# Kernel tuning notes

Hardware: AMD Instinct MI355X
Metric: run time of the kernel (lower is better)

The kernel has to match this reference:

```python
import jax, jax.numpy as jnp
import numpy as np

ATTN = 128

def _gelu(x):
    return jax.nn.gelu(x, approximate=False)

def _mlp3(x, W1, b1, W2, b2, W3, b3):
    h = _gelu(x @ W1.T + b1)
    h = _gelu(h @ W2.T + b2)
    return h @ W3.T + b3

def setup_inputs() -> dict:
    key = jax.random.key(0)
    ks = jax.random.split(key, 32)
    B, K, M, C = 128, 64, 2048, 32
    QD, AD, H = 128, 128, 256
    s = 0.02
    d = {}
    d['g'] = jax.random.normal(ks[0], (B, K, 3), dtype=jnp.float32)
    d['query'] = jax.random.normal(ks[1], (M, QD), dtype=jnp.float32) * s
    d['qW'] = jax.random.normal(ks[2], (AD, QD), dtype=jnp.float32) * s
    d['qb'] = jnp.zeros((AD,), jnp.float32)
    d['kW'] = jax.random.normal(ks[3], (AD, 1), dtype=jnp.float32) * s
    d['kb'] = jnp.zeros((AD,), jnp.float32)
    # global_mlp: K -> H -> H -> H
    d['gm_W1'] = jax.random.normal(ks[4], (H, K), dtype=jnp.float32) * s
    d['gm_b1'] = jnp.zeros((H,), jnp.float32)
    d['gm_W2'] = jax.random.normal(ks[5], (H, H), dtype=jnp.float32) * s
    d['gm_b2'] = jnp.zeros((H,), jnp.float32)
    d['gm_W3'] = jax.random.normal(ks[6], (H, H), dtype=jnp.float32) * s
    d['gm_b3'] = jnp.zeros((H,), jnp.float32)
    # point_mlp: (H+QD+1) -> H -> H -> H
    d['pm_W1'] = jax.random.normal(ks[7], (H, H + QD + 1), dtype=jnp.float32) * s
    d['pm_b1'] = jnp.zeros((H,), jnp.float32)
    d['pm_W2'] = jax.random.normal(ks[8], (H, H), dtype=jnp.float32) * s
    d['pm_b2'] = jnp.zeros((H,), jnp.float32)
    d['pm_W3'] = jax.random.normal(ks[9], (H, H), dtype=jnp.float32) * s
    d['pm_b3'] = jnp.zeros((H,), jnp.float32)
    d['tW'] = jax.random.normal(ks[10], (C, H), dtype=jnp.float32) * s
    d['tb'] = jnp.zeros((C,), jnp.float32)
    d['wW'] = jax.random.normal(ks[11], (1, H), dtype=jnp.float32) * s
    d['wb'] = jnp.zeros((1,), jnp.float32)
    d['cW'] = jax.random.normal(ks[12], (1, H), dtype=jnp.float32) * s
    d['cb'] = jnp.zeros((1,), jnp.float32)
    return d

def reference(g, query, qW, qb, kW, kb,
              gm_W1, gm_b1, gm_W2, gm_b2, gm_W3, gm_b3,
              pm_W1, pm_b1, pm_W2, pm_b2, pm_W3, pm_b3,
              tW, tb, wW, wb, cW, cb):
    B, K, _ = g.shape
    M = query.shape[0]
    inv = jnp.linalg.norm(g, axis=-1)                    # (B,K)
    Q = query @ qW.T + qb                                # (M,AD)
    Kk = inv[..., None] * kW[:, 0] + kb                  # (B,K,AD) Linear(1->AD)
    scores = jnp.einsum('md,bkd->bmk', Q, Kk) / jnp.sqrt(jnp.float32(Q.shape[-1]))
    A = jax.nn.softmax(scores, axis=-1)                  # (B,M,K)
    y = jnp.einsum('bmk,bkd->bmd', A, g)                 # (B,M,3)
    global_s = _mlp3(inv, gm_W1, gm_b1, gm_W2, gm_b2, gm_W3, gm_b3)  # (B,H)
    attended_inv = jnp.einsum('bmk,bk->bm', A, inv)      # (B,M)
    s_in = jnp.concatenate([
        jnp.broadcast_to(global_s[:, None, :], (B, M, global_s.shape[-1])),
        jnp.broadcast_to(query[None], (B, M, query.shape[-1])),
        attended_inv[..., None],
    ], axis=-1)                                          # (B,M,H+QD+1)
    s = _mlp3(s_in, pm_W1, pm_b1, pm_W2, pm_b2, pm_W3, pm_b3)  # (B,M,H)
    type_logits = s @ tW.T + tb                          # (B,M,C)
    weight_logits = (s @ wW.T + wb)[..., 0]              # (B,M)
    gate = jnp.clip(jax.nn.sigmoid(s @ cW.T + cb), 0.0, 1.0)  # (B,M,1)
    y = y * gate
    return (y, type_logits, weight_logits)
```

## Files before the change

kernel.cpp:

```cpp
#include <hip/hip_runtime.h>
#include <hip/hip_bf16.h>
#include <math.h>


typedef __attribute__((ext_vector_type(8))) short short8;
typedef __attribute__((ext_vector_type(4))) float f32x4;

__device__ __forceinline__ unsigned short bf16_rne(float f){
    union { float f; unsigned u; } v; v.f = f;
    return (unsigned short)((v.u + 0x7FFFu + ((v.u >> 16) & 1u)) >> 16);
}
__device__ __forceinline__ unsigned pk_bf16(float a, float b){
    float2 t; t.x = a; t.y = b;
    __hip_bfloat162 h = __float22bfloat162_rn(t);
    union { __hip_bfloat162 h; unsigned u; } cv; cv.h = h;
    return cv.u;
}
__device__ __forceinline__ short8 cvt8_f4(const float* __restrict__ p){
    float4 a = *(const float4*)p;
    float4 b = *(const float4*)(p + 4);
    short8 s;
    s[0]=(short)bf16_rne(a.x); s[1]=(short)bf16_rne(a.y);
    s[2]=(short)bf16_rne(a.z); s[3]=(short)bf16_rne(a.w);
    s[4]=(short)bf16_rne(b.x); s[5]=(short)bf16_rne(b.y);
    s[6]=(short)bf16_rne(b.z); s[7]=(short)bf16_rne(b.w);
    return s;
}
__device__ __forceinline__ short8 cvt8_s(const float* __restrict__ p){
    short8 s;
    #pragma unroll
    for (int i = 0; i < 8; ++i) s[i] = (short)bf16_rne(p[i]);
    return s;
}

__device__ __forceinline__ float gelu_f(float x){
    float z  = x * 0.70710678118654752f;
    float az = fabsf(z);
    float t  = __builtin_amdgcn_rcpf(1.0f + 0.3275911f * az);
    float p  = t*(0.254829592f + t*(-0.284496736f + t*(1.421413741f + t*(-1.453152027f + t*1.061405429f))));
    float e  = __expf(-az*az);
    float er = copysignf(1.0f - p*e, z);
    return 0.5f * x * (1.0f + er);
}
__device__ __forceinline__ float gelu_fast(float x){
    float x2 = x*x;
    float p  = fmaf(x2, -0.1029433f, -2.3022082f);
    float u  = x*p;
    float e  = __builtin_amdgcn_exp2f(u);
    float r  = __builtin_amdgcn_rcpf(1.0f + e);
    return x*r;
}

__global__ __launch_bounds__(256)
void k_prep(const float* __restrict__ g, const float* __restrict__ qW,
            const float* __restrict__ qb, const float* __restrict__ kW,
            const float* __restrict__ query, const float* __restrict__ pmW1,
            const float* __restrict__ pmb1,
            const float* __restrict__ pmW2, const float* __restrict__ pmW3,
            const float* __restrict__ pmb3,
            const float* __restrict__ gmW1, const float* __restrict__ gmb1,
            const float* __restrict__ gmW2, const float* __restrict__ gmb2,
            const float* __restrict__ gmW3, const float* __restrict__ gmb3,
            const float* __restrict__ tW, const float* __restrict__ tb,
            const float* __restrict__ wW, const float* __restrict__ wb,
            const float* __restrict__ cW, const float* __restrict__ cb,
            float* __restrict__ invg, float* __restrict__ ag,
            float* __restrict__ u1g, float* __restrict__ u2g,
            unsigned short* __restrict__ w2b, unsigned short* __restrict__ wheadb,
            float* __restrict__ bheadg, float* __restrict__ w385g) {
    __shared__ __align__(16) unsigned char smem[87040];
    const int bid = blockIdx.x, tid = threadIdx.x;
    const int w = tid >> 6, lane = tid & 63, q = lane >> 4, ln = lane & 15;

    if (bid < 32) {
        int idx = bid*256 + tid;
        const float* p = g + idx*3;
        invg[idx] = sqrtf(p[0]*p[0] + p[1]*p[1] + p[2]*p[2]);
    } else if (bid < 96) {
        int o = (bid - 32)*1024 + tid*4;
        float4 x = *(const float4*)&pmW2[o];
        union { unsigned short u[4]; uint2 v; } r;
        r.u[0] = bf16_rne(x.x); r.u[1] = bf16_rne(x.y);
        r.u[2] = bf16_rne(x.z); r.u[3] = bf16_rne(x.w);
        *(uint2*)&w2b[o] = r.v;
    } else if (bid < 130) {
        float* hw = (float*)smem;
        int c = bid - 96;
        const float* src = (c < 32) ? (tW + c*256) : ((c == 32) ? wW : cW);
        hw[tid] = src[tid];
        __syncthreads();
        float acc = 0.f;
        for (int j = 0; j < 256; ++j) acc += hw[j] * pmW3[j*256 + tid];
        wheadb[c*256 + tid] = bf16_rne(acc);
        if (tid == 0) {
            float bacc = (c < 32) ? tb[c] : ((c == 32) ? wb[0] : cb[0]);
            for (int j = 0; j < 256; ++j) bacc += hw[j] * pmb3[j];
            bheadg[c] = bacc;
        }
    } else if (bid == 130) {
        w385g[tid] = pmW1[tid*385 + 384];
    } else if (bid < 139) {
        float* kws = (float*)smem;
        float* vs  = kws + 128;
        float* red = vs  + 128;
        if (tid < 128) kws[tid] = kW[tid];
        __syncthreads();
        if (tid < 128) {
            float acc = 0.f;
            for (int d = 0; d < 128; ++d) acc += qW[d*128 + tid] * kws[d];
            vs[tid] = acc;
            red[tid] = qb[tid] * kws[tid];
        }
        __syncthreads();
        float s0 = 0.f;
        #pragma unroll 8
        for (int i = 0; i < 128; ++i) s0 += red[i];
        int m = (bid - 131)*256 + tid;
        const float4* qp = (const float4*)(query + m*128);
        float acc = s0;
        #pragma unroll 8
        for (int e4 = 0; e4 < 32; ++e4) {
            float4 qv = qp[e4];
            acc += qv.x*vs[e4*4] + qv.y*vs[e4*4+1] + qv.z*vs[e4*4+2] + qv.w*vs[e4*4+3];
        }
        ag[m] = acc * 0.08838834764831845f;
    } else if (bid < 141) {
        unsigned short* invA = (unsigned short*)smem;
        unsigned short* hA   = (unsigned short*)(smem + 9216);
        unsigned short* hB   = (unsigned short*)(smem + 43008);
        const int b0 = (bid - 139)*64;
        for (int i = tid; i < 4096; i += 256) {
            int r = i >> 6, k = i & 63;
            const float* p = g + ((size_t)(b0 + r)*64 + k)*3;
            invA[r*72 + k] = bf16_rne(sqrtf(p[0]*p[0] + p[1]*p[1] + p[2]*p[2]));
        }
        __syncthreads();

        f32x4 acc[4][4];
        #pragma unroll
        for (int mt = 0; mt < 4; ++mt)
            #pragma unroll
            for (int nt = 0; nt < 4; ++nt) acc[mt][nt] = (f32x4){0.f,0.f,0.f,0.f};
        #pragma unroll
        for (int kk = 0; kk < 2; ++kk) {
            const int kc = kk*32 + q*8;
            short8 af[4], bf_[4];
            #pragma unroll
            for (int mt = 0; mt < 4; ++mt) af[mt] = *(const short8*)&invA[(mt*16 + ln)*72 + kc];
            #pragma unroll
            for (int nt = 0; nt < 4; ++nt) bf_[nt] = cvt8_f4(gmW1 + (w*64 + nt*16 + ln)*64 + kc);
            #pragma unroll
            for (int mt = 0; mt < 4; ++mt)
                #pragma unroll
                for (int nt = 0; nt < 4; ++nt)
                    acc[mt][nt] = __builtin_amdgcn_mfma_f32_16x16x32_bf16(af[mt], bf_[nt], acc[mt][nt], 0, 0, 0);
        }
        #pragma unroll
        for (int mt = 0; mt < 4; ++mt)
            #pragma unroll
            for (int nt = 0; nt < 4; ++nt) {
                const int n = w*64 + nt*16 + ln;
                const float bb = gmb1[n];
                #pragma unroll
                for (int rg = 0; rg < 4; ++rg)
                    hA[(mt*16 + q*4 + rg)*264 + n] = bf16_rne(gelu_f(acc[mt][nt][rg] + bb));
            }
        __syncthreads();
        #pragma unroll
        for (int mt = 0; mt < 4; ++mt)
            #pragma unroll
            for (int nt = 0; nt < 4; ++nt) acc[mt][nt] = (f32x4){0.f,0.f,0.f,0.f};
        for (int kk = 0; kk < 8; ++kk) {
            const int kc = kk*32 + q*8;
            short8 af[4], bf_[4];
            #pragma unroll
            for (int mt = 0; mt < 4; ++mt) af[mt] = *(const short8*)&hA[(mt*16 + ln)*264 + kc];
            #pragma unroll
            for (int nt = 0; nt < 4; ++nt) bf_[nt] = cvt8_f4(gmW2 + (w*64 + nt*16 + ln)*256 + kc);
            #pragma unroll
            for (int mt = 0; mt < 4; ++mt)
                #pragma unroll
                for (int nt = 0; nt < 4; ++nt)
                    acc[mt][nt] = __builtin_amdgcn_mfma_f32_16x16x32_bf16(af[mt], bf_[nt], acc[mt][nt], 0, 0, 0);
        }
        __syncthreads();
        #pragma unroll
        for (int mt = 0; mt < 4; ++mt)
            #pragma unroll
            for (int nt = 0; nt < 4; ++nt) {
                const int n = w*64 + nt*16 + ln;
                const float bb = gmb2[n];
                #pragma unroll
                for (int rg = 0; rg < 4; ++rg)
                    hB[(mt*16 + q*4 + rg)*264 + n] = bf16_rne(gelu_f(acc[mt][nt][rg] + bb));
            }
        __syncthreads();
        #pragma unroll
        for (int mt = 0; mt < 4; ++mt)
            #pragma unroll
            for (int nt = 0; nt < 4; ++nt) acc[mt][nt] = (f32x4){0.f,0.f,0.f,0.f};
        for (int kk = 0; kk < 8; ++kk) {
            const int kc = kk*32 + q*8;
            short8 af[4], bf_[4];
            #pragma unroll
            for (int mt = 0; mt < 4; ++mt) af[mt] = *(const short8*)&hB[(mt*16 + ln)*264 + kc];
            #pragma unroll
            for (int nt = 0; nt < 4; ++nt) bf_[nt] = cvt8_f4(gmW3 + (w*64 + nt*16 + ln)*256 + kc);
            #pragma unroll
            for (int mt = 0; mt < 4; ++mt)
                #pragma unroll
                for (int nt = 0; nt < 4; ++nt)
                    acc[mt][nt] = __builtin_amdgcn_mfma_f32_16x16x32_bf16(af[mt], bf_[nt], acc[mt][nt], 0, 0, 0);
        }
        __syncthreads();
        #pragma unroll
        for (int mt = 0; mt < 4; ++mt)
            #pragma unroll
            for (int nt = 0; nt < 4; ++nt) {
                const int n = w*64 + nt*16 + ln;
                const float bb = gmb3[n];
                #pragma unroll
                for (int rg = 0; rg < 4; ++rg)
                    hA[(mt*16 + q*4 + rg)*264 + n] = bf16_rne(acc[mt][nt][rg] + bb);
            }
        __syncthreads();
        #pragma unroll
        for (int mt = 0; mt < 4; ++mt)
            #pragma unroll
            for (int nt = 0; nt < 4; ++nt) acc[mt][nt] = (f32x4){0.f,0.f,0.f,0.f};
        for (int kk = 0; kk < 8; ++kk) {
            const int kc = kk*32 + q*8;
            short8 af[4], bf_[4];
            #pragma unroll
            for (int mt = 0; mt < 4; ++mt) af[mt] = *(const short8*)&hA[(mt*16 + ln)*264 + kc];
            #pragma unroll
            for (int nt = 0; nt < 4; ++nt) bf_[nt] = cvt8_s(pmW1 + (size_t)(w*64 + nt*16 + ln)*385 + kc);
            #pragma unroll
            for (int mt = 0; mt < 4; ++mt)
                #pragma unroll
                for (int nt = 0; nt < 4; ++nt)
                    acc[mt][nt] = __builtin_amdgcn_mfma_f32_16x16x32_bf16(af[mt], bf_[nt], acc[mt][nt], 0, 0, 0);
        }
        #pragma unroll
        for (int mt = 0; mt < 4; ++mt)
            #pragma unroll
            for (int nt = 0; nt < 4; ++nt) {
                const int n = w*64 + nt*16 + ln;
                const float bb = pmb1[n];
                #pragma unroll
                for (int rg = 0; rg < 4; ++rg)
                    u1g[(size_t)(b0 + mt*16 + q*4 + rg)*256 + n] = acc[mt][nt][rg] + bb;
            }
    } else {
        unsigned short* qs = (unsigned short*)smem;
        unsigned short* wsd = (unsigned short*)(smem + 17408);
        const int m0 = (bid - 141)*64;
        for (int i = tid; i < 64*128; i += 256) {
            int r = i >> 7, c = i & 127;
            qs[r*136 + c] = bf16_rne(query[(size_t)(m0 + r)*128 + c]);
        }
        for (int i = tid; i < 256*128; i += 256) {
            int n = i >> 7, c = i & 127;
            wsd[n*136 + c] = bf16_rne(pmW1[(size_t)n*385 + 256 + c]);
        }
        __syncthreads();
        f32x4 acc[4][4];
        #pragma unroll
        for (int mt = 0; mt < 4; ++mt)
            #pragma unroll
            for (int nt = 0; nt < 4; ++nt) acc[mt][nt] = (f32x4){0.f,0.f,0.f,0.f};
        #pragma unroll
        for (int kk = 0; kk < 4; ++kk) {
            const int kc = kk*32 + q*8;
            short8 af[4], bf_[4];
            #pragma unroll
            for (int mt = 0; mt < 4; ++mt) af[mt] = *(const short8*)&qs[(mt*16 + ln)*136 + kc];
            #pragma unroll
            for (int nt = 0; nt < 4; ++nt) bf_[nt] = *(const short8*)&wsd[(w*64 + nt*16 + ln)*136 + kc];
            #pragma unroll
            for (int mt = 0; mt < 4; ++mt)
                #pragma unroll
                for (int nt = 0; nt < 4; ++nt)
                    acc[mt][nt] = __builtin_amdgcn_mfma_f32_16x16x32_bf16(af[mt], bf_[nt], acc[mt][nt], 0, 0, 0);
        }
        #pragma unroll
        for (int mt = 0; mt < 4; ++mt)
            #pragma unroll
            for (int nt = 0; nt < 4; ++nt) {
                const int n = w*64 + nt*16 + ln;
                #pragma unroll
                for (int rg = 0; rg < 4; ++rg)
                    u2g[(size_t)(m0 + mt*16 + q*4 + rg)*256 + n] = acc[mt][nt][rg];
            }
    }
}

__global__ __launch_bounds__(256, 4)
void k_main(const float* __restrict__ g,
            const float* __restrict__ invg, const float* __restrict__ ag,
            const float* __restrict__ u1g, const float* __restrict__ u2g,
            const float* __restrict__ w385g, const float* __restrict__ pmb2,
            const unsigned short* __restrict__ w2b, const unsigned short* __restrict__ wheadb,
            const float* __restrict__ bheadg, float* __restrict__ out) {
    __shared__ __align__(16) unsigned short hb[64*264];
    __shared__ __align__(16) float u1s[256], w385s[256], pmb2s[256];
    __shared__ float invs[64], gsl[192], ainv_s[64], y0s[192];

    const int tid = threadIdx.x;
    const int bid = blockIdx.x;
    const int b  = bid >> 5;
    const int m0 = (bid & 31) << 6;

    if (tid < 64)  invs[tid] = invg[b*64 + tid];
    if (tid < 192) gsl[tid]  = g[b*192 + tid];
    u1s[tid]   = u1g[b*256 + tid];
    w385s[tid] = w385g[tid];
    pmb2s[tid] = pmb2[tid];
    __syncthreads();

    {
        const int r = tid >> 2, sub = tid & 3;
        const float am = ag[m0 + r];
        const int kb = sub * 16;
        float mx = -1e30f;
        #pragma unroll
        for (int i = 0; i < 16; ++i) mx = fmaxf(mx, invs[kb + i] * am);
        #pragma unroll
        for (int d = 1; d < 4; d <<= 1) mx = fmaxf(mx, __shfl_xor(mx, d, 64));
        float den = 0.f, ai = 0.f, y0 = 0.f, y1 = 0.f, y2 = 0.f;
        #pragma unroll
        for (int i = 0; i < 16; ++i) {
            const int k = kb + i;
            const float iv = invs[k];
            const float e = __expf(iv * am - mx);
            den += e; ai += e * iv;
            y0 += e * gsl[k*3+0]; y1 += e * gsl[k*3+1]; y2 += e * gsl[k*3+2];
        }
        #pragma unroll
        for (int d = 1; d < 4; d <<= 1) {
            den += __shfl_xor(den, d, 64);
            ai  += __shfl_xor(ai , d, 64);
            y0  += __shfl_xor(y0 , d, 64);
            y1  += __shfl_xor(y1 , d, 64);
            y2  += __shfl_xor(y2 , d, 64);
        }
        if (sub == 0) {
            const float id = 1.0f / den;
            ainv_s[r] = ai * id;
            y0s[r*3+0] = y0*id; y0s[r*3+1] = y1*id; y0s[r*3+2] = y2*id;
        }
    }
    __syncthreads();

    {
        const int ln16 = tid & 15, rbase = tid >> 4;
        #pragma unroll
        for (int rr = 0; rr < 4; ++rr) {
            const int r = rr*16 + rbase;
            const float aiv = ainv_s[r];
            const float* u2p = u2g + (size_t)(m0 + r)*256;
            #pragma unroll
            for (int k = 0; k < 4; ++k) {
                const int c = ln16*4 + k*64;
                float4 x  = *(const float4*)&u2p[c];
                float4 uv = *(const float4*)&u1s[c];
                float4 wv = *(const float4*)&w385s[c];
                float g0 = gelu_fast(x.x + uv.x + aiv*wv.x);
                float g1 = gelu_fast(x.y + uv.y + aiv*wv.y);
                float g2 = gelu_fast(x.z + uv.z + aiv*wv.z);
                float g3 = gelu_fast(x.w + uv.w + aiv*wv.w);
                uint2 pk; pk.x = pk_bf16(g0, g1); pk.y = pk_bf16(g2, g3);
                *(uint2*)&hb[r*264 + c] = pk;
            }
        }
    }
    __syncthreads();

    const int w = tid >> 6, lane = tid & 63;
    const int q = lane >> 4, ln = lane & 15;

    f32x4 acc[4][4];
    #pragma unroll
    for (int mt = 0; mt < 4; ++mt)
        #pragma unroll
        for (int nt = 0; nt < 4; ++nt) acc[mt][nt] = (f32x4){0.f,0.f,0.f,0.f};

    {
        const unsigned short* w2p = w2b + (w*64 + ln)*256 + q*8;
        short8 bcur[4], bnxt[4];
        #pragma unroll
        for (int nt = 0; nt < 4; ++nt) bcur[nt] = *(const short8*)(w2p + nt*4096);
        #pragma unroll
        for (int kk = 0; kk < 8; ++kk) {
            if (kk < 7) {
                #pragma unroll
                for (int nt = 0; nt < 4; ++nt)
                    bnxt[nt] = *(const short8*)(w2p + nt*4096 + (kk+1)*32);
            }
            short8 afrag[4];
            const int kc = kk*32 + q*8;
            #pragma unroll
            for (int mt = 0; mt < 4; ++mt)
                afrag[mt] = *(const short8*)&hb[(mt*16 + ln)*264 + kc];
            #pragma unroll
            for (int mt = 0; mt < 4; ++mt)
                #pragma unroll
                for (int nt = 0; nt < 4; ++nt)
                    acc[mt][nt] = __builtin_amdgcn_mfma_f32_16x16x32_bf16(afrag[mt], bcur[nt], acc[mt][nt], 0, 0, 0);
            #pragma unroll
            for (int nt = 0; nt < 4; ++nt) bcur[nt] = bnxt[nt];
        }
    }
    __syncthreads();

    #pragma unroll
    for (int mt = 0; mt < 4; ++mt) {
        #pragma unroll
        for (int nt = 0; nt < 4; ++nt) {
            const int n = w*64 + nt*16 + ln;
            const float bb = pmb2s[n];
            const int r0 = mt*16 + q*4;
            float h0 = gelu_fast(acc[mt][nt][0] + bb);
            float h1 = gelu_fast(acc[mt][nt][1] + bb);
            float h2 = gelu_fast(acc[mt][nt][2] + bb);
            float h3 = gelu_fast(acc[mt][nt][3] + bb);
            unsigned p01 = pk_bf16(h0, h1);
            unsigned p23 = pk_bf16(h2, h3);
            hb[(r0+0)*264 + n] = (unsigned short)(p01 & 0xFFFF);
            hb[(r0+1)*264 + n] = (unsigned short)(p01 >> 16);
            hb[(r0+2)*264 + n] = (unsigned short)(p23 & 0xFFFF);
            hb[(r0+3)*264 + n] = (unsigned short)(p23 >> 16);
        }
    }

    const int cb2 = (ln < 2) ? (32 + ln) : 33;
    const unsigned short* whp = wheadb + q*8;
    short8 wf0 = *(const short8*)(whp +  ln      *256);
    short8 wf1 = *(const short8*)(whp + (16 + ln)*256);
    short8 wf2 = *(const short8*)(whp +  cb2     *256);
    __syncthreads();

    f32x4 accA0 = {0.f,0.f,0.f,0.f}, accA1 = {0.f,0.f,0.f,0.f}, accB = {0.f,0.f,0.f,0.f};
    const int rr = w*16 + ln;
    #pragma unroll
    for (int kk = 0; kk < 8; ++kk) {
        short8 wn0, wn1, wn2;
        if (kk < 7) {
            wn0 = *(const short8*)(whp +  ln      *256 + (kk+1)*32);
            wn1 = *(const short8*)(whp + (16 + ln)*256 + (kk+1)*32);
            wn2 = *(const short8*)(whp +  cb2     *256 + (kk+1)*32);
        }
        short8 bh = *(const short8*)&hb[rr*264 + kk*32 + q*8];
        accA0 = __builtin_amdgcn_mfma_f32_16x16x32_bf16(wf0, bh, accA0, 0, 0, 0);
        accA1 = __builtin_amdgcn_mfma_f32_16x16x32_bf16(wf1, bh, accA1, 0, 0, 0);
        accB  = __builtin_amdgcn_mfma_f32_16x16x32_bf16(wf2, bh, accB , 0, 0, 0);
        wf0 = wn0; wf1 = wn1; wf2 = wn2;
    }
    {
        const size_t row = (size_t)b*2048 + m0 + rr;
        const int c0 = q*4;
        f32x4 r0 = accA0 + *(const f32x4*)&bheadg[c0];
        f32x4 r1 = accA1 + *(const f32x4*)&bheadg[16 + c0];
        *(f32x4*)&out[786432 + row*32 + c0]      = r0;
        *(f32x4*)&out[786432 + row*32 + 16 + c0] = r1;
        if (q == 0) {
            out[9175040 + row] = accB[0] + bheadg[32];
            float gv = accB[1] + bheadg[33];
            float gt = 1.0f / (1.0f + __expf(-gv));
            gt = fminf(fmaxf(gt, 0.0f), 1.0f);
            float* yo = out + row*3;
            yo[0] = y0s[rr*3+0] * gt;
            yo[1] = y0s[rr*3+1] * gt;
            yo[2] = y0s[rr*3+2] * gt;
        }
    }
}

extern "C" void kernel_launch(void* const* d_in, const int* in_sizes, int n_in,
                              void* d_out, int out_size, void* d_ws, size_t ws_size,
                              hipStream_t stream) {
    const float* g     = (const float*)d_in[0];
    const float* query = (const float*)d_in[1];
    const float* qW    = (const float*)d_in[2];
    const float* qb    = (const float*)d_in[3];
    const float* kW    = (const float*)d_in[4];
    const float* gmW1  = (const float*)d_in[6];
    const float* gmb1  = (const float*)d_in[7];
    const float* gmW2  = (const float*)d_in[8];
    const float* gmb2  = (const float*)d_in[9];
    const float* gmW3  = (const float*)d_in[10];
    const float* gmb3  = (const float*)d_in[11];
    const float* pmW1  = (const float*)d_in[12];
    const float* pmb1  = (const float*)d_in[13];
    const float* pmW2  = (const float*)d_in[14];
    const float* pmb2  = (const float*)d_in[15];
    const float* pmW3  = (const float*)d_in[16];
    const float* pmb3  = (const float*)d_in[17];
    const float* tW    = (const float*)d_in[18];
    const float* tb    = (const float*)d_in[19];
    const float* wW    = (const float*)d_in[20];
    const float* wb    = (const float*)d_in[21];
    const float* cW    = (const float*)d_in[22];
    const float* cb    = (const float*)d_in[23];
    float* out = (float*)d_out;

    float* ws    = (float*)d_ws;
    float* invg  = ws;
    float* ag    = ws + 8192;
    float* u1g   = ws + 10240;
    float* w385g = ws + 43008;
    float* bheadg= ws + 43264;
    unsigned short* w2b    = (unsigned short*)(ws + 43328);
    unsigned short* wheadb = (unsigned short*)(ws + 76096);
    float* u2g   = ws + 80448;

    hipLaunchKernelGGL(k_prep, dim3(173), dim3(256), 0, stream,
                       g, qW, qb, kW, query, pmW1, pmb1, pmW2, pmW3, pmb3,
                       gmW1, gmb1, gmW2, gmb2, gmW3, gmb3,
                       tW, tb, wW, wb, cW, cb,
                       invg, ag, u1g, u2g, w2b, wheadb, bheadg, w385g);
    hipLaunchKernelGGL(k_main, dim3(4096), dim3(256), 0, stream,
                       g, invg, ag, u1g, u2g, w385g, pmb2,
                       w2b, wheadb, bheadg, out);
}
```

Before: 255.4 us.

## Stage pmW1 in LDS, swap GEMM operands for packed stores, use polynomial GELU

Three changes at once. The pm_W1 projection in the prep kernel now stages bf16-converted weight chunks in shared memory with coalesced loads, instead of doing strided scalar global loads per fragment. The main layer-2 GEMM swaps the A and B operands so each lane's accumulator holds four consecutive output columns, which lets the GELU epilogue write packed 8-byte stores instead of four scalar 2-byte stores. The sigmoid-based GELU approximation is replaced by a clamped Taylor polynomial of Phi with no exp or rcp, which is cheaper but less accurate for large |x| and adds extra barriers in the prep kernel.

```diff
diff --git a/kernel.cpp b/kernel.cpp
--- a/kernel.cpp
+++ b/kernel.cpp
@@ -26,12 +26,6 @@
     s[6]=(short)bf16_rne(b.z); s[7]=(short)bf16_rne(b.w);
     return s;
 }
-__device__ __forceinline__ short8 cvt8_s(const float* __restrict__ p){
-    short8 s;
-    #pragma unroll
-    for (int i = 0; i < 8; ++i) s[i] = (short)bf16_rne(p[i]);
-    return s;
-}
 
 __device__ __forceinline__ float gelu_f(float x){
     float z  = x * 0.70710678118654752f;
@@ -42,13 +36,14 @@
     float er = copysignf(1.0f - p*e, z);
     return 0.5f * x * (1.0f + er);
 }
-__device__ __forceinline__ float gelu_fast(float x){
-    float x2 = x*x;
-    float p  = fmaf(x2, -0.1029433f, -2.3022082f);
-    float u  = x*p;
-    float e  = __builtin_amdgcn_exp2f(u);
-    float r  = __builtin_amdgcn_rcpf(1.0f + e);
-    return x*r;
+__device__ __forceinline__ float gelu_poly(float x){
+    float t = x*x;
+    float p = fmaf(t, -2.9761905e-3f, 2.5e-2f);
+    p = fmaf(t, p, -0.16666667f);
+    p = fmaf(t, p, 1.0f);
+    float Phi = fmaf(x*p, 0.39894228f, 0.5f);
+    Phi = fminf(fmaxf(Phi, 0.0f), 1.0f);
+    return x * Phi;
 }
 
 __global__ __launch_bounds__(256)
@@ -223,23 +218,33 @@
                 for (int rg = 0; rg < 4; ++rg)
                     hA[(mt*16 + q*4 + rg)*264 + n] = bf16_rne(acc[mt][nt][rg] + bb);
             }
-        __syncthreads();
+        unsigned short* w1s = (unsigned short*)(smem + 43008);
         #pragma unroll
         for (int mt = 0; mt < 4; ++mt)
             #pragma unroll
             for (int nt = 0; nt < 4; ++nt) acc[mt][nt] = (f32x4){0.f,0.f,0.f,0.f};
-        for (int kk = 0; kk < 8; ++kk) {
-            const int kc = kk*32 + q*8;
-            short8 af[4], bf_[4];
-            #pragma unroll
-            for (int mt = 0; mt < 4; ++mt) af[mt] = *(const short8*)&hA[(mt*16 + ln)*264 + kc];
-            #pragma unroll
-            for (int nt = 0; nt < 4; ++nt) bf_[nt] = cvt8_s(pmW1 + (size_t)(w*64 + nt*16 + ln)*385 + kc);
-            #pragma unroll
-            for (int mt = 0; mt < 4; ++mt)
-                #pragma unroll
-                for (int nt = 0; nt < 4; ++nt)
-                    acc[mt][nt] = __builtin_amdgcn_mfma_f32_16x16x32_bf16(af[mt], bf_[nt], acc[mt][nt], 0, 0, 0);
+        for (int chunk = 0; chunk < 4; ++chunk) {
+            __syncthreads();
+            for (int i = tid; i < 256*64; i += 256) {
+                int n = i >> 6, c = i & 63;
+                w1s[n*72 + c] = bf16_rne(pmW1[(size_t)n*385 + chunk*64 + c]);
+            }
+            __syncthreads();
+            #pragma unroll
+            for (int kk2 = 0; kk2 < 2; ++kk2) {
+                const int kl = kk2*32 + q*8;
+                const int kg = chunk*64 + kl;
+                short8 af[4], bf_[4];
+                #pragma unroll
+                for (int mt = 0; mt < 4; ++mt) af[mt] = *(const short8*)&hA[(mt*16 + ln)*264 + kg];
+                #pragma unroll
+                for (int nt = 0; nt < 4; ++nt) bf_[nt] = *(const short8*)&w1s[(w*64 + nt*16 + ln)*72 + kl];
+                #pragma unroll
+                for (int mt = 0; mt < 4; ++mt)
+                    #pragma unroll
+                    for (int nt = 0; nt < 4; ++nt)
+                        acc[mt][nt] = __builtin_amdgcn_mfma_f32_16x16x32_bf16(af[mt], bf_[nt], acc[mt][nt], 0, 0, 0);
+            }
         }
         #pragma unroll
         for (int mt = 0; mt < 4; ++mt)
@@ -365,10 +370,10 @@
                 float4 x  = *(const float4*)&u2p[c];
                 float4 uv = *(const float4*)&u1s[c];
                 float4 wv = *(const float4*)&w385s[c];
-                float g0 = gelu_fast(x.x + uv.x + aiv*wv.x);
-                float g1 = gelu_fast(x.y + uv.y + aiv*wv.y);
-                float g2 = gelu_fast(x.z + uv.z + aiv*wv.z);
-                float g3 = gelu_fast(x.w + uv.w + aiv*wv.w);
+                float g0 = gelu_poly(x.x + uv.x + aiv*wv.x);
+                float g1 = gelu_poly(x.y + uv.y + aiv*wv.y);
+                float g2 = gelu_poly(x.z + uv.z + aiv*wv.z);
+                float g3 = gelu_poly(x.w + uv.w + aiv*wv.w);
                 uint2 pk; pk.x = pk_bf16(g0, g1); pk.y = pk_bf16(g2, g3);
                 *(uint2*)&hb[r*264 + c] = pk;
             }
@@ -381,55 +386,51 @@
 
     f32x4 acc[4][4];
     #pragma unroll
-    for (int mt = 0; mt < 4; ++mt)
-        #pragma unroll
-        for (int nt = 0; nt < 4; ++nt) acc[mt][nt] = (f32x4){0.f,0.f,0.f,0.f};
+    for (int a = 0; a < 4; ++a)
+        #pragma unroll
+        for (int c = 0; c < 4; ++c) acc[a][c] = (f32x4){0.f,0.f,0.f,0.f};
 
     {
         const unsigned short* w2p = w2b + (w*64 + ln)*256 + q*8;
-        short8 bcur[4], bnxt[4];
-        #pragma unroll
-        for (int nt = 0; nt < 4; ++nt) bcur[nt] = *(const short8*)(w2p + nt*4096);
+        short8 acur[4], anxt[4];
+        #pragma unroll
+        for (int a = 0; a < 4; ++a) acur[a] = *(const short8*)(w2p + a*4096);
         #pragma unroll
         for (int kk = 0; kk < 8; ++kk) {
             if (kk < 7) {
                 #pragma unroll
-                for (int nt = 0; nt < 4; ++nt)
-                    bnxt[nt] = *(const short8*)(w2p + nt*4096 + (kk+1)*32);
-            }
-            short8 afrag[4];
+                for (int a = 0; a < 4; ++a)
+                    anxt[a] = *(const short8*)(w2p + a*4096 + (kk+1)*32);
+            }
+            short8 bfrag[4];
             const int kc = kk*32 + q*8;
             #pragma unroll
-            for (int mt = 0; mt < 4; ++mt)
-                afrag[mt] = *(const short8*)&hb[(mt*16 + ln)*264 + kc];
-            #pragma unroll
-            for (int mt = 0; mt < 4; ++mt)
-                #pragma unroll
-                for (int nt = 0; nt < 4; ++nt)
-                    acc[mt][nt] = __builtin_amdgcn_mfma_f32_16x16x32_bf16(afrag[mt], bcur[nt], acc[mt][nt], 0, 0, 0);
-            #pragma unroll
-            for (int nt = 0; nt < 4; ++nt) bcur[nt] = bnxt[nt];
+            for (int c = 0; c < 4; ++c)
+                bfrag[c] = *(const short8*)&hb[(c*16 + ln)*264 + kc];
+            #pragma unroll
+            for (int a = 0; a < 4; ++a)
+                #pragma unroll
+                for (int c = 0; c < 4; ++c)
+                    acc[a][c] = __builtin_amdgcn_mfma_f32_16x16x32_bf16(acur[a], bfrag[c], acc[a][c], 0, 0, 0);
+            #pragma unroll
+            for (int a = 0; a < 4; ++a) acur[a] = anxt[a];
         }
     }
     __syncthreads();
 
     #pragma unroll
-    for (int mt = 0; mt < 4; ++mt) {
-        #pragma unroll
-        for (int nt = 0; nt < 4; ++nt) {
-            const int n = w*64 + nt*16 + ln;
-            const float bb = pmb2s[n];
-            const int r0 = mt*16 + q*4;
-            float h0 = gelu_fast(acc[mt][nt][0] + bb);
-            float h1 = gelu_fast(acc[mt][nt][1] + bb);
-            float h2 = gelu_fast(acc[mt][nt][2] + bb);
-            float h3 = gelu_fast(acc[mt][nt][3] + bb);
-            unsigned p01 = pk_bf16(h0, h1);
-            unsigned p23 = pk_bf16(h2, h3);
-            hb[(r0+0)*264 + n] = (unsigned short)(p01 & 0xFFFF);
-            hb[(r0+1)*264 + n] = (unsigned short)(p01 >> 16);
-            hb[(r0+2)*264 + n] = (unsigned short)(p23 & 0xFFFF);
-            hb[(r0+3)*264 + n] = (unsigned short)(p23 >> 16);
+    for (int a = 0; a < 4; ++a) {
+        const int n0 = w*64 + a*16 + q*4;
+        const float4 bb4 = *(const float4*)&pmb2s[n0];
+        #pragma unroll
+        for (int c = 0; c < 4; ++c) {
+            const int m = c*16 + ln;
+            float h0 = gelu_poly(acc[a][c][0] + bb4.x);
+            float h1 = gelu_poly(acc[a][c][1] + bb4.y);
+            float h2 = gelu_poly(acc[a][c][2] + bb4.z);
+            float h3 = gelu_poly(acc[a][c][3] + bb4.w);
+            uint2 pk2; pk2.x = pk_bf16(h0, h1); pk2.y = pk_bf16(h2, h3);
+            *(uint2*)&hb[m*264 + n0] = pk2;
         }
     }
 
```

Measured after the change: 259.1 us. No clear change (+1.5%).
